# Performance work log

Measured on AMD Instinct MI355X. Metric: run time of the kernel, lower is better.

## Reference

```python
import jax, jax.numpy as jnp
import numpy as np


def setup_inputs() -> dict:
    key = jax.random.key(0)
    k1, k2, k3 = jax.random.split(key, 3)
    B, N, D = 512, 12, 4
    return {
        "x": jax.random.normal(k1, (B, N), dtype=jnp.float32),
        "rys": jax.random.normal(k2, (D, N), dtype=jnp.float32),
        "cnot_params": jax.random.normal(k3, (D, N - 1), dtype=jnp.float32),
    }


def _rx(state, theta, q, B):
    # RX(theta) = [[c, -i s], [-i s, c]], half-angle; theta: (B,)
    s = state.reshape(B, 2 ** q, 2, -1)
    c = jnp.cos(theta * 0.5)[:, None, None].astype(state.dtype)
    sn = (-1j * jnp.sin(theta * 0.5))[:, None, None].astype(state.dtype)
    a0, a1 = s[:, :, 0], s[:, :, 1]
    return jnp.stack([c * a0 + sn * a1, sn * a0 + c * a1], axis=2).reshape(B, -1)


def _ry(state, theta, q, B):
    # RY(theta) = [[c, -s], [s, c]], half-angle; theta: scalar (shared over batch)
    s = state.reshape(B, 2 ** q, 2, -1)
    c = jnp.cos(theta * 0.5).astype(state.dtype)
    sn = jnp.sin(theta * 0.5).astype(state.dtype)
    a0, a1 = s[:, :, 0], s[:, :, 1]
    return jnp.stack([c * a0 - sn * a1, sn * a0 + c * a1], axis=2).reshape(B, -1)


def _cnot(state, q, B):
    # CNOT on adjacent wires (control=q, target=q+1): flip target where control=1
    s = state.reshape(B, 2 ** q, 2, 2, -1)
    return jnp.stack([s[:, :, 0], s[:, :, 1, ::-1]], axis=2).reshape(B, -1)


def reference(x, rys, cnot_params):
    B, n = x.shape
    depth = rys.shape[0]
    # wire 0 is the most-significant bit (PennyLane convention)
    state = jnp.zeros((B, 2 ** n), dtype=jnp.complex64).at[:, 0].set(1.0)
    for q in range(n):
        state = _rx(state, x[:, q], q, B)
    for d in range(depth):
        for q in range(n):
            state = _ry(state, rys[d, q], q, B)
        for q in range(n - 1):  # cnot_params are declared but unused (CNOT is non-parametric)
            state = _cnot(state, q, B)
    probs = jnp.abs(state) ** 2  # (B, 2^n), real
    zs = []
    for q in range(n):
        p = probs.reshape(B, 2 ** q, 2, -1).sum(axis=(1, 3))  # (B, 2)
        zs.append(p[:, 0] - p[:, 1])
    return jnp.stack(zs, axis=1).astype(jnp.float32)  # (B, n)
```

## Files before the change

### kernel.cpp

```cpp
#include <hip/hip_runtime.h>

#define NQ 12
#define DIM 4096
#define BLK 256

typedef float v2f __attribute__((ext_vector_type(2)));

__host__ __device__ constexpr int igrayc(int v) {
    v ^= v >> 1; v ^= v >> 2; v ^= v >> 4; v ^= v >> 8;
    return v & (DIM - 1);
}
__host__ __device__ constexpr int gkf(int v, int k) {
    if (k == 1) v ^= v >> 1;
    else if (k == 2) v ^= v >> 2;
    else { v ^= v >> 2; v ^= v >> 1; }
    return v;
}
__host__ __device__ constexpr int sigf(int v) { return v ^ ((v >> 4) & 15); }
__host__ __device__ constexpr int TkF(int v, int k) { return sigf(gkf(v, k)); }

__device__ __forceinline__ v2f cmul(v2f a, v2f b) {
    v2f r; r.x = a.x * b.x - a.y * b.y; r.y = a.x * b.y + a.y * b.x; return r;
}
__device__ __forceinline__ void gate_pair(v2f& a0, v2f& a1, v2f cc, v2f ss, v2f ns) {
    v2f t0 = a0, t1 = a1;
    a0 = __builtin_elementwise_fma(ns, t1, cc * t0);
    a1 = __builtin_elementwise_fma(ss, t0, cc * t1);
}
template<int PB>
__device__ __forceinline__ void gate16(v2f (&a)[16], float c, float s) {
    const v2f cc = {c, c}, ss = {s, s}, ns = {-s, -s};
    #pragma unroll
    for (int j0 = 0; j0 < 16; ++j0) {
        if (j0 & PB) continue;
        gate_pair(a[j0], a[j0 | PB], cc, ss, ns);
    }
}

template<int CTRL, int BETA>
__device__ __forceinline__ void dpp_gate16(v2f (&a)[16], float c, float s, int lb) {
    const float sl = ((lb >> BETA) & 1) ? s : -s;
    const v2f cc = {c, c}, sv = {sl, sl};
    #pragma unroll
    for (int j = 0; j < 16; ++j) {
        int bx = __builtin_amdgcn_update_dpp(0, __float_as_int(a[j].x), CTRL, 0xf, 0xf, true);
        int by = __builtin_amdgcn_update_dpp(0, __float_as_int(a[j].y), CTRL, 0xf, 0xf, true);
        v2f b; b.x = __int_as_float(bx); b.y = __int_as_float(by);
        a[j] = __builtin_elementwise_fma(sv, b, cc * a[j]);
    }
}
#define DPP_XOR1  0xB1
#define DPP_XOR2  0x4E
#define DPP_XOR7  0x141
#define DPP_XOR15 0x140

template<int K, int OSH>
__device__ __forceinline__ void ld16(const char* bufc, int sb8, v2f (&a)[16]) {
    #pragma unroll
    for (int j = 0; j < 16; ++j)
        a[j] = *(const v2f*)(bufc + (sb8 ^ (TkF(j << OSH, K) << 3)));
}
template<int K, int OSH>
__device__ __forceinline__ void st16(char* bufc, int sb8, const v2f (&a)[16]) {
    #pragma unroll
    for (int j = 0; j < 16; ++j)
        *(v2f*)(bufc + (sb8 ^ (TkF(j << OSH, K) << 3))) = a[j];
}

__device__ __forceinline__ float wave64_sum(float v) {
    v += __int_as_float(__builtin_amdgcn_update_dpp(0, __float_as_int(v), 0x111, 0xf, 0xf, true));
    v += __int_as_float(__builtin_amdgcn_update_dpp(0, __float_as_int(v), 0x112, 0xf, 0xf, true));
    v += __int_as_float(__builtin_amdgcn_update_dpp(0, __float_as_int(v), 0x114, 0xf, 0xf, true));
    v += __int_as_float(__builtin_amdgcn_update_dpp(0, __float_as_int(v), 0x118, 0xf, 0xf, true));
    v += __int_as_float(__builtin_amdgcn_update_dpp(0, __float_as_int(v), 0x142, 0xa, 0xf, false));
    v += __int_as_float(__builtin_amdgcn_update_dpp(0, __float_as_int(v), 0x143, 0xc, 0xf, false));
    return v;
}

__global__ __launch_bounds__(BLK, 2)
void qsim_kernel(const float* __restrict__ x,
                 const float* __restrict__ rys,
                 float* __restrict__ out) {
    __shared__ __align__(16) v2f buf[DIM];
    __shared__ float cr[4 * NQ], sr[4 * NQ];
    __shared__ v2f fac[NQ][2];
    __shared__ float zred[4][NQ];

    const int b = blockIdx.x;
    const int t = threadIdx.x;
    char* bufc = (char*)buf;

    if (t < 4 * NQ) {
        float th = 0.5f * rys[t];
        cr[t] = cosf(th); sr[t] = sinf(th);
    }
    if (t >= 64 && t < 64 + NQ) {
        int q = t - 64;
        float xh = 0.5f * x[b * NQ + q];
        float cx = cosf(xh), sx = sinf(xh);
        float th = 0.5f * rys[q];
        float c0 = cosf(th), s0 = sinf(th);
        int p = NQ - 1 - q;
        fac[p][0] = v2f{c0 * cx,  s0 * sx};
        fac[p][1] = v2f{s0 * cx, -c0 * sx};
    }
    __syncthreads();

    const int lb = (t & 3) ^ (((t >> 2) & 1) * 7) ^ (((t >> 3) & 1) * 12)
                 ^ ((t >> 4) << 8);

    {
        v2f a[16];
        const int Mb = t ^ (t >> 1);
        v2f P = fac[0][Mb & 1];
        #pragma unroll
        for (int p = 1; p < 7; ++p) P = cmul(P, fac[p][(Mb >> p) & 1]);
        const int b7 = (Mb >> 7) & 1;
        v2f E = cmul(P, fac[7][b7]);
        v2f O = cmul(P, fac[7][b7 ^ 1]);
        v2f L4[4], H4[4];
        #pragma unroll
        for (int v = 0; v < 4; ++v) {
            L4[v] = cmul(fac[8][v & 1],  fac[9][(v >> 1) & 1]);
            H4[v] = cmul(fac[10][v & 1], fac[11][(v >> 1) & 1]);
        }
        #pragma unroll
        for (int j = 0; j < 16; ++j) {
            const int gv = (j ^ (j >> 1)) & 15;
            a[j] = cmul((j & 1) ? O : E, cmul(L4[gv & 3], H4[(gv >> 2) & 3]));
        }
        gate16<1>(a, cr[15], sr[15]);
        gate16<2>(a, cr[14], sr[14]);
        gate16<4>(a, cr[13], sr[13]);
        gate16<8>(a, cr[12], sr[12]);
        st16<1, 8>(bufc, TkF(t, 1) << 3, a);
    }
    __syncthreads();

    #define AB_PASS(K, D)                                          \
    {                                                              \
        const int sb8 = TkF(lb, K) << 3;                           \
        v2f a[16];                                                 \
        ld16<K, 4>(bufc, sb8, a);                                  \
        gate16<1>(a, cr[(D)*NQ + 7], sr[(D)*NQ + 7]);              \
        gate16<2>(a, cr[(D)*NQ + 6], sr[(D)*NQ + 6]);              \
        gate16<4>(a, cr[(D)*NQ + 5], sr[(D)*NQ + 5]);              \
        gate16<8>(a, cr[(D)*NQ + 4], sr[(D)*NQ + 4]);              \
        dpp_gate16<DPP_XOR1,  0>(a, cr[(D)*NQ + 11], sr[(D)*NQ + 11], lb); \
        dpp_gate16<DPP_XOR2,  1>(a, cr[(D)*NQ + 10], sr[(D)*NQ + 10], lb); \
        dpp_gate16<DPP_XOR7,  2>(a, cr[(D)*NQ + 9],  sr[(D)*NQ + 9],  lb); \
        dpp_gate16<DPP_XOR15, 3>(a, cr[(D)*NQ + 8],  sr[(D)*NQ + 8],  lb); \
        st16<K, 4>(bufc, sb8, a);                                  \
    }                                                              \
    __syncthreads();

    #define C_PASS(K, I0, I1, I2, I3)                              \
    {                                                              \
        const int sb8 = TkF(t, K) << 3;                            \
        v2f a[16];                                                 \
        ld16<K, 8>(bufc, sb8, a);                                  \
        gate16<1>(a, cr[I0], sr[I0]);                              \
        gate16<2>(a, cr[I1], sr[I1]);                              \
        gate16<4>(a, cr[I2], sr[I2]);                              \
        gate16<8>(a, cr[I3], sr[I3]);                              \
        st16<K, 8>(bufc, sb8, a);                                  \
    }                                                              \
    __syncthreads();

    AB_PASS(1, 1)
    C_PASS(2, 27, 26, 25, 24)
    AB_PASS(2, 2)
    C_PASS(3, 39, 38, 37, 36)
    #undef AB_PASS
    #undef C_PASS

    {
        const int sb8 = TkF(lb, 3) << 3;
        v2f a[16];
        ld16<3, 4>(bufc, sb8, a);
        gate16<1>(a, cr[43], sr[43]);
        gate16<2>(a, cr[42], sr[42]);
        gate16<4>(a, cr[41], sr[41]);
        gate16<8>(a, cr[40], sr[40]);
        dpp_gate16<DPP_XOR1,  0>(a, cr[47], sr[47], lb);
        dpp_gate16<DPP_XOR2,  1>(a, cr[46], sr[46], lb);
        dpp_gate16<DPP_XOR7,  2>(a, cr[45], sr[45], lb);
        dpp_gate16<DPP_XOR15, 3>(a, cr[44], sr[44], lb);

        float pr[16];
        #pragma unroll
        for (int j = 0; j < 16; ++j)
            pr[j] = a[j].x * a[j].x + a[j].y * a[j].y;
        #pragma unroll
        for (int bit = 1; bit < 16; bit <<= 1) {
            #pragma unroll
            for (int j = 0; j < 16; ++j) {
                if (j & bit) continue;
                float u = pr[j], w = pr[j | bit];
                pr[j] = u + w;
                pr[j | bit] = u - w;
            }
        }
        const int R = igrayc(lb);
        #pragma unroll
        for (int q = 0; q < NQ; ++q) {
            const int l = NQ - 1 - q;
            const float cf = (l <= 4) ? pr[15]
                           : (l == 5) ? pr[14]
                           : (l == 6) ? pr[12]
                           : (l == 7) ? pr[8]  : pr[0];
            float v = ((R >> l) & 1) ? -cf : cf;
            v = wave64_sum(v);
            if ((t & 63) == 63) zred[t >> 6][q] = v;
        }
    }
    __syncthreads();
    if (t < NQ)
        out[b * NQ + t] = zred[0][t] + zred[1][t] + zred[2][t] + zred[3][t];
}

extern "C" void kernel_launch(void* const* d_in, const int* in_sizes, int n_in,
                              void* d_out, int out_size, void* d_ws, size_t ws_size,
                              hipStream_t stream) {
    const float* x   = (const float*)d_in[0];
    const float* rys = (const float*)d_in[1];
    float* out = (float*)d_out;
    qsim_kernel<<<512, BLK, 0, stream>>>(x, rys, out);
}
```

Before: 16.74 us.

## Fuse initial product state with first AB pass and merge passes to cut barriers

Builds the initial product state directly in the register layout used by the first AB pass and applies that pass's gates before the first shared-memory store, removing one load/store round trip and one barrier. The first C pass of the next layer is merged with the leftover wire-15 gate through a custom shared-memory layout (c1off), with a DPP-based gate and hand-permuted gate pairs. The kernel now has fewer LDS passes and __syncthreads, in exchange for more intricate index mappings that must exactly match the earlier layout.

New measurement: 16.91 us. No clear change (+1.0%).

```diff
diff --git a/kernel.cpp b/kernel.cpp
--- a/kernel.cpp
+++ b/kernel.cpp
@@ -18,6 +18,11 @@
 }
 __host__ __device__ constexpr int sigf(int v) { return v ^ ((v >> 4) & 15); }
 __host__ __device__ constexpr int TkF(int v, int k) { return sigf(gkf(v, k)); }
+
+__host__ __device__ constexpr int c1off(int j) {
+    return ((j & 1) ? 0x188 : 0) ^ ((j & 2) ? 0x300 : 0)
+         ^ ((j & 4) ? 0x600 : 0) ^ ((j & 8) ? 0xC00 : 0);
+}
 
 __device__ __forceinline__ v2f cmul(v2f a, v2f b) {
     v2f r; r.x = a.x * b.x - a.y * b.y; r.y = a.x * b.y + a.y * b.x; return r;
@@ -110,69 +115,143 @@
                  ^ ((t >> 4) << 8);
 
     {
+        const int m0 = (t ^ (t >> 1)) & 1;
+        const int m1 = ((t >> 1) ^ (t >> 3)) & 1;
+        const int m2 = (t >> 2) & 1;
+        const int t3b = (t >> 3) & 1, t4b = (t >> 4) & 1;
+        const int m8 = ((t >> 4) ^ (t >> 5)) & 1;
+        const int m9 = ((t >> 5) ^ (t >> 6)) & 1;
+        const int m10 = ((t >> 6) ^ (t >> 7)) & 1;
+        const int m11 = (t >> 7) & 1;
+        v2f U = cmul(cmul(cmul(fac[0][m0], fac[1][m1]), cmul(fac[2][m2], fac[8][m8])),
+                     cmul(cmul(fac[9][m9], fac[10][m10]), fac[11][m11]));
+        v2f f3[2] = {fac[3][t3b], fac[3][t3b ^ 1]};
+        v2f f4[2] = {fac[4][0], fac[4][1]};
+        v2f f5[2] = {fac[5][0], fac[5][1]};
+        v2f f6[2] = {fac[6][0], fac[6][1]};
+        v2f f7[2] = {fac[7][t4b], fac[7][t4b ^ 1]};
+
+        v2f T7[2], T6[4], T5[8], a[16];
+        #pragma unroll
+        for (int j3 = 0; j3 < 2; ++j3) T7[j3] = cmul(U, f7[j3]);
+        #pragma unroll
+        for (int h = 0; h < 4; ++h) {
+            int j2 = h & 1, j3 = h >> 1;
+            T6[h] = cmul(T7[j3], f6[j2 ^ j3]);
+        }
+        #pragma unroll
+        for (int h = 0; h < 8; ++h) {
+            int j1 = h & 1, j2 = (h >> 1) & 1;
+            T5[h] = cmul(T6[h >> 1], f5[j1 ^ j2]);
+        }
+        #pragma unroll
+        for (int j = 0; j < 16; ++j) {
+            int j0 = j & 1, j1 = (j >> 1) & 1;
+            v2f A = cmul(T5[j >> 1], f4[j0 ^ j1]);
+            a[j] = cmul(A, f3[j0]);
+        }
+        gate16<1>(a, cr[19], sr[19]);
+        gate16<2>(a, cr[18], sr[18]);
+        gate16<4>(a, cr[17], sr[17]);
+        gate16<8>(a, cr[16], sr[16]);
+        dpp_gate16<DPP_XOR1,  0>(a, cr[23], sr[23], lb);
+        dpp_gate16<DPP_XOR2,  1>(a, cr[22], sr[22], lb);
+        dpp_gate16<DPP_XOR7,  2>(a, cr[21], sr[21], lb);
+        dpp_gate16<DPP_XOR15, 3>(a, cr[20], sr[20], lb);
+        st16<1, 4>(bufc, TkF(lb, 1) << 3, a);
+    }
+    __syncthreads();
+
+    {
+        const int sb8 = ((t & ~4) ^ (((t >> 2) & 1) * 0x147)) << 3;
         v2f a[16];
-        const int Mb = t ^ (t >> 1);
-        v2f P = fac[0][Mb & 1];
-        #pragma unroll
-        for (int p = 1; p < 7; ++p) P = cmul(P, fac[p][(Mb >> p) & 1]);
-        const int b7 = (Mb >> 7) & 1;
-        v2f E = cmul(P, fac[7][b7]);
-        v2f O = cmul(P, fac[7][b7 ^ 1]);
-        v2f L4[4], H4[4];
-        #pragma unroll
-        for (int v = 0; v < 4; ++v) {
-            L4[v] = cmul(fac[8][v & 1],  fac[9][(v >> 1) & 1]);
-            H4[v] = cmul(fac[10][v & 1], fac[11][(v >> 1) & 1]);
-        }
-        #pragma unroll
-        for (int j = 0; j < 16; ++j) {
-            const int gv = (j ^ (j >> 1)) & 15;
-            a[j] = cmul((j & 1) ? O : E, cmul(L4[gv & 3], H4[(gv >> 2) & 3]));
-        }
-        gate16<1>(a, cr[15], sr[15]);
+        #pragma unroll
+        for (int j = 0; j < 16; ++j)
+            a[j] = *(const v2f*)(bufc + (sb8 ^ (c1off(j) << 3)));
+
+        {
+            float c = cr[15], s = sr[15];
+            float swf = ((t >> 2) & 1) ? s : -s;
+            v2f cc = {c, c}, sw = {swf, swf}, nsw = {-swf, -swf};
+            #pragma unroll
+            for (int j = 0; j < 16; j += 2) {
+                v2f u = a[j], v = a[j + 1];
+                a[j]     = __builtin_elementwise_fma(sw, v, cc * u);
+                a[j + 1] = __builtin_elementwise_fma(nsw, u, cc * v);
+            }
+        }
         gate16<2>(a, cr[14], sr[14]);
         gate16<4>(a, cr[13], sr[13]);
         gate16<8>(a, cr[12], sr[12]);
-        st16<1, 8>(bufc, TkF(t, 1) << 3, a);
-    }
-    __syncthreads();
-
-    #define AB_PASS(K, D)                                          \
-    {                                                              \
-        const int sb8 = TkF(lb, K) << 3;                           \
-        v2f a[16];                                                 \
-        ld16<K, 4>(bufc, sb8, a);                                  \
-        gate16<1>(a, cr[(D)*NQ + 7], sr[(D)*NQ + 7]);              \
-        gate16<2>(a, cr[(D)*NQ + 6], sr[(D)*NQ + 6]);              \
-        gate16<4>(a, cr[(D)*NQ + 5], sr[(D)*NQ + 5]);              \
-        gate16<8>(a, cr[(D)*NQ + 4], sr[(D)*NQ + 4]);              \
-        dpp_gate16<DPP_XOR1,  0>(a, cr[(D)*NQ + 11], sr[(D)*NQ + 11], lb); \
-        dpp_gate16<DPP_XOR2,  1>(a, cr[(D)*NQ + 10], sr[(D)*NQ + 10], lb); \
-        dpp_gate16<DPP_XOR7,  2>(a, cr[(D)*NQ + 9],  sr[(D)*NQ + 9],  lb); \
-        dpp_gate16<DPP_XOR15, 3>(a, cr[(D)*NQ + 8],  sr[(D)*NQ + 8],  lb); \
-        st16<K, 4>(bufc, sb8, a);                                  \
-    }                                                              \
-    __syncthreads();
-
-    #define C_PASS(K, I0, I1, I2, I3)                              \
-    {                                                              \
-        const int sb8 = TkF(t, K) << 3;                            \
-        v2f a[16];                                                 \
-        ld16<K, 8>(bufc, sb8, a);                                  \
-        gate16<1>(a, cr[I0], sr[I0]);                              \
-        gate16<2>(a, cr[I1], sr[I1]);                              \
-        gate16<4>(a, cr[I2], sr[I2]);                              \
-        gate16<8>(a, cr[I3], sr[I3]);                              \
-        st16<K, 8>(bufc, sb8, a);                                  \
-    }                                                              \
-    __syncthreads();
-
-    AB_PASS(1, 1)
-    C_PASS(2, 27, 26, 25, 24)
-    AB_PASS(2, 2)
-    C_PASS(3, 39, 38, 37, 36)
-    #undef AB_PASS
-    #undef C_PASS
+
+        {
+            float c = cr[27], s = sr[27];
+            float bs = ((t >> 2) & 1) ? s : -s;
+            v2f cc = {c, c};
+            #pragma unroll
+            for (int j = 0; j < 16; ++j) {
+                float slf = (__builtin_popcount(j) & 1) ? -bs : bs;
+                v2f sv = {slf, slf};
+                int bx = __builtin_amdgcn_update_dpp(0, __float_as_int(a[j].x), DPP_XOR7, 0xf, 0xf, true);
+                int by = __builtin_amdgcn_update_dpp(0, __float_as_int(a[j].y), DPP_XOR7, 0xf, 0xf, true);
+                v2f p; p.x = __int_as_float(bx); p.y = __int_as_float(by);
+                a[j] = __builtin_elementwise_fma(sv, p, cc * a[j]);
+            }
+        }
+        {
+            const v2f cc = {cr[26], cr[26]}, ss = {sr[26], sr[26]}, ns = {-sr[26], -sr[26]};
+            gate_pair(a[0], a[3], cc, ss, ns);   gate_pair(a[1], a[2], cc, ss, ns);
+            gate_pair(a[7], a[4], cc, ss, ns);   gate_pair(a[6], a[5], cc, ss, ns);
+            gate_pair(a[11], a[8], cc, ss, ns);  gate_pair(a[10], a[9], cc, ss, ns);
+            gate_pair(a[12], a[15], cc, ss, ns); gate_pair(a[13], a[14], cc, ss, ns);
+        }
+        {
+            const v2f cc = {cr[25], cr[25]}, ss = {sr[25], sr[25]}, ns = {-sr[25], -sr[25]};
+            gate_pair(a[0], a[6], cc, ss, ns);   gate_pair(a[1], a[7], cc, ss, ns);
+            gate_pair(a[2], a[4], cc, ss, ns);   gate_pair(a[3], a[5], cc, ss, ns);
+            gate_pair(a[14], a[8], cc, ss, ns);  gate_pair(a[15], a[9], cc, ss, ns);
+            gate_pair(a[12], a[10], cc, ss, ns); gate_pair(a[13], a[11], cc, ss, ns);
+        }
+        {
+            const v2f cc = {cr[24], cr[24]}, ss = {sr[24], sr[24]}, ns = {-sr[24], -sr[24]};
+            gate_pair(a[0], a[12], cc, ss, ns);  gate_pair(a[1], a[13], cc, ss, ns);
+            gate_pair(a[2], a[14], cc, ss, ns);  gate_pair(a[3], a[15], cc, ss, ns);
+            gate_pair(a[4], a[8], cc, ss, ns);   gate_pair(a[5], a[9], cc, ss, ns);
+            gate_pair(a[6], a[10], cc, ss, ns);  gate_pair(a[7], a[11], cc, ss, ns);
+        }
+        #pragma unroll
+        for (int j = 0; j < 16; ++j)
+            *(v2f*)(bufc + (sb8 ^ (c1off(j) << 3))) = a[j];
+    }
+    __syncthreads();
+
+    {
+        const int sb8 = TkF(lb, 2) << 3;
+        v2f a[16];
+        ld16<2, 4>(bufc, sb8, a);
+        gate16<1>(a, cr[31], sr[31]);
+        gate16<2>(a, cr[30], sr[30]);
+        gate16<4>(a, cr[29], sr[29]);
+        gate16<8>(a, cr[28], sr[28]);
+        dpp_gate16<DPP_XOR1,  0>(a, cr[35], sr[35], lb);
+        dpp_gate16<DPP_XOR2,  1>(a, cr[34], sr[34], lb);
+        dpp_gate16<DPP_XOR7,  2>(a, cr[33], sr[33], lb);
+        dpp_gate16<DPP_XOR15, 3>(a, cr[32], sr[32], lb);
+        st16<2, 4>(bufc, sb8, a);
+    }
+    __syncthreads();
+
+    {
+        const int sb8 = TkF(t, 3) << 3;
+        v2f a[16];
+        ld16<3, 8>(bufc, sb8, a);
+        gate16<1>(a, cr[39], sr[39]);
+        gate16<2>(a, cr[38], sr[38]);
+        gate16<4>(a, cr[37], sr[37]);
+        gate16<8>(a, cr[36], sr[36]);
+        st16<3, 8>(bufc, sb8, a);
+    }
+    __syncthreads();
 
     {
         const int sb8 = TkF(lb, 3) << 3;
```
